# Performance work log

Measured on AMD Instinct MI355X. Metric: run time of the kernel, lower is better.

The kernel has to match this reference:

```python
import jax, jax.numpy as jnp
import numpy as np

N, IN, C, H = 16384, 64, 4, 16
MAXS = 16  # upper bound on squaring steps (norms here give s ~ 7-8)


def setup_inputs() -> dict:
    key = jax.random.key(0)
    k1, k2, k3 = jax.random.split(key, 3)
    dX = jax.random.normal(k1, (N, IN), dtype=jnp.float32)
    Ar = jax.random.normal(k2, (IN, C, H, H), dtype=jnp.float32)
    Ai = jax.random.normal(k3, (IN, C, H, H), dtype=jnp.float32)
    return {"dX": dX, "Ar": Ar, "Ai": Ai}


def reference(dX, Ar, Ai):
    # Parameter A as complex64, projected onto the unitary Lie algebra (skew-Hermitian)
    A = (Ar + 1j * Ai).astype(jnp.complex64)
    A = (A - jnp.conj(jnp.swapaxes(A, -2, -1))) * 0.5  # (IN, C, H, H)
    # AX[n,c,i,j] = sum_k A[k,c,i,j] * dX[n,k]  -> (N, C, H, H)
    AX = jnp.einsum('kcij,nk->ncij', A, dX.astype(jnp.complex64))
    # induced 1-norm: max over columns of column abs-sums
    normA = jnp.max(jnp.sum(jnp.abs(AX), axis=-2), axis=-1)  # (N, C), real
    s = jnp.where(normA > 1, jnp.ceil(jnp.log2(normA)), 0.0).astype(jnp.int32)
    # scaling: exp(A) = exp(A / 2^s) ^ (2^s); integer s detaches grad like torch .long()
    scale = jnp.exp2(-s.astype(jnp.float32)).astype(jnp.complex64)[..., None, None]
    A1 = AX * scale
    n, c, h, _ = A1.shape
    P = jax.vmap(jax.scipy.linalg.expm)(A1.reshape(-1, h, h)).reshape(n, c, h, h)
    # repeated squaring, masked per (n, c) element; fixed trip count for jit
    for i in range(MAXS):
        P = jnp.where((s > i)[..., None, None], P @ P, P)
    return P
```

## Files before the change

### kernel.cpp

```cpp
#include <hip/hip_runtime.h>
#include <math.h>

#define NN       16384
#define IN_DIM   64
#define CC       4
#define NMAT     (NN * CC)

#define C0 1.0f
#define C1 1.0f
#define C2 0.5f
#define C3 0.16666666666666666f
#define C4 0.041666666666666664f
#define C5 0.008333333333333333f
#define C6 0.001388888888888889f
#define C7 1.984126984126984e-4f
#define C8 2.48015873015873e-5f

typedef __attribute__((ext_vector_type(8))) short bf16x8;
typedef __attribute__((ext_vector_type(4))) float f32x4;

#define MFMA16(A, B, C) __builtin_amdgcn_mfma_f32_16x16x32_bf16((A), (B), (C), 0, 0, 0)

#define COLP   768
#define ROWB   3072
#define MATB   6144
#define WPB    4

__device__ __forceinline__ unsigned hi16(float x) {
    return __builtin_bit_cast(unsigned, x) >> 16;
}
__device__ __forceinline__ float hif(float x) {
    return __builtin_bit_cast(float, __builtin_bit_cast(unsigned, x) & 0xFFFF0000u);
}
__device__ __forceinline__ unsigned pk2(float a, float b) {
    return (__builtin_bit_cast(unsigned, a) >> 16) |
           (__builtin_bit_cast(unsigned, b) & 0xFFFF0000u);
}

__global__ __launch_bounds__(256)
void ax_kernel(const float* __restrict__ dX, const float* __restrict__ Ar,
               const float* __restrict__ Ai, float* __restrict__ ws)
{
    const int t  = threadIdx.x;
    const int nb = blockIdx.x * 8;
    const int c  = t >> 6;
    const int i  = (t >> 2) & 15;
    const int j0 = (t & 3) * 4;

    float accre[8][4], accim[8][4];
#pragma unroll
    for (int nn_ = 0; nn_ < 8; ++nn_)
#pragma unroll
        for (int jj = 0; jj < 4; ++jj) { accre[nn_][jj] = 0.f; accim[nn_][jj] = 0.f; }

#pragma unroll 2
    for (int k = 0; k < IN_DIM; ++k) {
        const int base = (k * CC + c) * 256 + i * 16 + j0;
        const float4 ar = *reinterpret_cast<const float4*>(Ar + base);
        const float4 ai = *reinterpret_cast<const float4*>(Ai + base);
#pragma unroll
        for (int nn_ = 0; nn_ < 8; ++nn_) {
            const float dxv = dX[(nb + nn_) * IN_DIM + k];
#pragma unroll
            for (int jj = 0; jj < 4; ++jj) {
                accre[nn_][jj] = fmaf(dxv, (&ar.x)[jj], accre[nn_][jj]);
                accim[nn_][jj] = fmaf(dxv, (&ai.x)[jj], accim[nn_][jj]);
            }
        }
    }
#pragma unroll
    for (int nn_ = 0; nn_ < 8; ++nn_) {
        const int m = (nb + nn_) * CC + c;
        float* o = ws + (size_t)m * 512 + (i * 16 + j0) * 2;
        reinterpret_cast<float4*>(o)[0] =
            make_float4(accre[nn_][0], accim[nn_][0], accre[nn_][1], accim[nn_][1]);
        reinterpret_cast<float4*>(o)[1] =
            make_float4(accre[nn_][2], accim[nn_][2], accre[nn_][3], accim[nn_][3]);
    }
}

__global__ __launch_bounds__(256)
void expm_mfma_kernel(const float* __restrict__ dX, const float* __restrict__ Ar,
                      const float* __restrict__ Ai, const float* __restrict__ ws,
                      float* __restrict__ out, const int use_ws, const int real_only)
{
    __shared__ __align__(16) unsigned char ldsraw[WPB * MATB];

    const int t = threadIdx.x;
    const int w = t >> 6;
    const int l = t & 63;
    unsigned char* L = ldsraw + w * MATB;

    const int m  = blockIdx.x * WPB + w;
    const int n  = m >> 2;
    const int cc = m & 3;

    const int c     = l & 15;
    const int g     = l >> 4;
    const int ghalf = g & 1;
    const int gsel  = g >> 1;

    const int colent  = c * 48 + ghalf * 16;
    const int off_B1h = (gsel ? COLP : 0) + colent;
    const int off_B2h = (gsel ? 0 : COLP) + colent;
    const int off_Ah  = ROWB + (gsel ? COLP : 0) + colent;
    const int wc      = c * 48 + g * 8;

    const short ns = gsel ? (short)0x8000 : (short)0;
    const bf16x8 negv = {ns, ns, ns, ns, ns, ns, ns, ns};

    float dq[4];
#pragma unroll
    for (int q = 0; q < 4; ++q) dq[q] = ((4 * g + q) == c) ? 1.f : 0.f;

    float aRe[4], aIm[4];
    if (use_ws) {
        const float* gp = ws + (size_t)m * 512;
#pragma unroll
        for (int q = 0; q < 4; ++q) {
            const int r = 4 * g + q;
            const float2 v = *reinterpret_cast<const float2*>(gp + (r * 16 + c) * 2);
            const float2 u = *reinterpret_cast<const float2*>(gp + (c * 16 + r) * 2);
            aRe[q] = 0.5f * (v.x - u.x);
            aIm[q] = 0.5f * (v.y + u.y);
        }
    } else {
        float bRe[4] = {0,0,0,0}, bIm[4] = {0,0,0,0}, uRe[4] = {0,0,0,0}, uIm[4] = {0,0,0,0};
        for (int k = 0; k < IN_DIM; ++k) {
            const float dxv = dX[n * IN_DIM + k];
            const int base = (k * CC + cc) * 256;
#pragma unroll
            for (int q = 0; q < 4; ++q) {
                const int r = 4 * g + q;
                bRe[q] = fmaf(dxv, Ar[base + r * 16 + c], bRe[q]);
                bIm[q] = fmaf(dxv, Ai[base + r * 16 + c], bIm[q]);
                uRe[q] = fmaf(dxv, Ar[base + c * 16 + r], uRe[q]);
                uIm[q] = fmaf(dxv, Ai[base + c * 16 + r], uIm[q]);
            }
        }
#pragma unroll
        for (int q = 0; q < 4; ++q) {
            aRe[q] = 0.5f * (bRe[q] - uRe[q]);
            aIm[q] = 0.5f * (bIm[q] + uIm[q]);
        }
    }

    float colsum = 0.f;
#pragma unroll
    for (int q = 0; q < 4; ++q)
        colsum += sqrtf(aRe[q] * aRe[q] + aIm[q] * aIm[q]);
    colsum += __shfl_xor(colsum, 16);
    colsum += __shfl_xor(colsum, 32);
    float mx = colsum;
    mx = fmaxf(mx, __shfl_xor(mx, 1));
    mx = fmaxf(mx, __shfl_xor(mx, 2));
    mx = fmaxf(mx, __shfl_xor(mx, 4));
    mx = fmaxf(mx, __shfl_xor(mx, 8));

    int s = 0;
    if (mx > 1.f) s = (int)ceilf(log2f(mx));
    if (s < 0) s = 0;
    if (s > 16) s = 16;
    const float sc = exp2f((float)(-s));
#pragma unroll
    for (int q = 0; q < 4; ++q) { aRe[q] *= sc; aIm[q] *= sc; }

    auto wcol = [&](const float* vR, const float* vI) {
        uint2 xh, yh, xl, yl;
        xh.x = pk2(vR[0], vR[1]); xh.y = pk2(vR[2], vR[3]);
        yh.x = pk2(vI[0], vI[1]); yh.y = pk2(vI[2], vI[3]);
        float l0 = vR[0] - hif(vR[0]), l1 = vR[1] - hif(vR[1]);
        float l2 = vR[2] - hif(vR[2]), l3 = vR[3] - hif(vR[3]);
        xl.x = pk2(l0, l1); xl.y = pk2(l2, l3);
        l0 = vI[0] - hif(vI[0]); l1 = vI[1] - hif(vI[1]);
        l2 = vI[2] - hif(vI[2]); l3 = vI[3] - hif(vI[3]);
        yl.x = pk2(l0, l1); yl.y = pk2(l2, l3);
        *reinterpret_cast<uint2*>(L + 0    + wc) = xh;
        *reinterpret_cast<uint2*>(L + COLP + wc) = yh;
        *reinterpret_cast<uint2*>(L + 1536 + wc) = xl;
        *reinterpret_cast<uint2*>(L + 2304 + wc) = yl;
    };
    auto wrow = [&](const float* vR, const float* vI) {
#pragma unroll
        for (int q = 0; q < 4; ++q) {
            const int rb = ROWB + (4 * g + q) * 48 + c * 2;
            *reinterpret_cast<unsigned short*>(L + rb + 0)    = (unsigned short)hi16(vR[q]);
            *reinterpret_cast<unsigned short*>(L + rb + COLP) = (unsigned short)hi16(vI[q]);
            const float lr = vR[q] - hif(vR[q]);
            const float li = vI[q] - hif(vI[q]);
            *reinterpret_cast<unsigned short*>(L + rb + 1536) = (unsigned short)hi16(lr);
            *reinterpret_cast<unsigned short*>(L + rb + 2304) = (unsigned short)hi16(li);
        }
    };
    auto cmul = [&](const bf16x8 Ah, const bf16x8 Al, f32x4& accRe, f32x4& accIm) {
        bf16x8 b1h = *reinterpret_cast<const bf16x8*>(L + off_B1h);
        bf16x8 b1l = *reinterpret_cast<const bf16x8*>(L + off_B1h + 1536);
        const bf16x8 b2h = *reinterpret_cast<const bf16x8*>(L + off_B2h);
        const bf16x8 b2l = *reinterpret_cast<const bf16x8*>(L + off_B2h + 1536);
        b1h ^= negv;
        b1l ^= negv;
        accRe = MFMA16(Ah, b1h, accRe);
        accRe = MFMA16(Ah, b1l, accRe);
        accRe = MFMA16(Al, b1h, accRe);
        accIm = MFMA16(Ah, b2h, accIm);
        accIm = MFMA16(Ah, b2l, accIm);
        accIm = MFMA16(Al, b2h, accIm);
    };

    wcol(aRe, aIm);
    wrow(aRe, aIm);
    bf16x8 Ah = *reinterpret_cast<const bf16x8*>(L + off_Ah);
    bf16x8 Al = *reinterpret_cast<const bf16x8*>(L + off_Ah + 1536);
    f32x4 zr4 = {0.f, 0.f, 0.f, 0.f}, zi4 = {0.f, 0.f, 0.f, 0.f};
    cmul(Ah, Al, zr4, zi4);

    float zr[4], zi[4];
#pragma unroll
    for (int q = 0; q < 4; ++q) { zr[q] = zr4[q]; zi[q] = zi4[q]; }
    wrow(zr, zi);
    const bf16x8 ZAh = *reinterpret_cast<const bf16x8*>(L + off_Ah);
    const bf16x8 ZAl = *reinterpret_cast<const bf16x8*>(L + off_Ah + 1536);

    float tRe[4], tIm[4];
#pragma unroll
    for (int q = 0; q < 4; ++q) {
        tRe[q] = C8 * zr[q] + C7 * aRe[q] + C6 * dq[q];
        tIm[q] = C8 * zi[q] + C7 * aIm[q];
    }

    const float cE[3] = {C4, C2, C0};
    const float cO[3] = {C5, C3, C1};
#pragma unroll
    for (int h = 0; h < 3; ++h) {
        wcol(tRe, tIm);
        f32x4 rr, ri;
#pragma unroll
        for (int q = 0; q < 4; ++q) {
            rr[q] = cO[h] * aRe[q] + cE[h] * dq[q];
            ri[q] = cO[h] * aIm[q];
        }
        cmul(ZAh, ZAl, rr, ri);
#pragma unroll
        for (int q = 0; q < 4; ++q) { tRe[q] = rr[q]; tIm[q] = ri[q]; }
    }

#pragma unroll 1
    for (int it = 0; it < s; ++it) {
        wcol(tRe, tIm);
        wrow(tRe, tIm);
        const bf16x8 Ph = *reinterpret_cast<const bf16x8*>(L + off_Ah);
        const bf16x8 Pl = *reinterpret_cast<const bf16x8*>(L + off_Ah + 1536);
        f32x4 rr = {0.f, 0.f, 0.f, 0.f}, ri = {0.f, 0.f, 0.f, 0.f};
        cmul(Ph, Pl, rr, ri);
#pragma unroll
        for (int q = 0; q < 4; ++q) { tRe[q] = rr[q]; tIm[q] = ri[q]; }
    }

    if (real_only) {
        float* po = out + (size_t)m * 256;
#pragma unroll
        for (int q = 0; q < 4; ++q)
            po[(4 * g + q) * 16 + c] = tRe[q];
    } else {
        float* po = out + (size_t)m * 512;
#pragma unroll
        for (int q = 0; q < 4; ++q)
            *reinterpret_cast<float2*>(po + ((4 * g + q) * 16 + c) * 2) =
                make_float2(tRe[q], tIm[q]);
    }
}

extern "C" void kernel_launch(void* const* d_in, const int* in_sizes, int n_in,
                              void* d_out, int out_size, void* d_ws, size_t ws_size,
                              hipStream_t stream)
{
    const float* dX = (const float*)d_in[0];
    const float* Ar = (const float*)d_in[1];
    const float* Ai = (const float*)d_in[2];
    float* out = (float*)d_out;
    float* ws  = (float*)d_ws;

    const int real_only = (out_size < NMAT * 512) ? 1 : 0;
    const size_t need = (size_t)NMAT * 512 * sizeof(float);
    const int use_ws = (ws_size >= need) ? 1 : 0;

    if (use_ws)
        hipLaunchKernelGGL(ax_kernel, dim3(NN / 8), dim3(256), 0, stream, dX, Ar, Ai, ws);
    hipLaunchKernelGGL(expm_mfma_kernel, dim3(NMAT / WPB), dim3(256), 0, stream,
                       dX, Ar, Ai, ws, out, use_ws, real_only);
}
```

Baseline: 258.3 us.

## Replace LDS operand staging with wave shuffles and track conjugate-transpose for squaring

Removes the per-wave LDS buffer. MFMA A/B operands are now built with cross-lane shuffles from register-packed bf16 hi/lo pieces. Because the input is skew-Hermitian, the kernel also evaluates the Taylor polynomial at -A to get exp(A)^H. During squaring it keeps both P and P^H so each operand comes from the right layout without a transpose through memory. This doubles the polynomial MFMA work and adds many shuffles and selects per step, in exchange for removing LDS stores, loads and bank traffic. It also skips the imaginary part on the last step when only real output is needed.

```diff
diff --git a/kernel.cpp b/kernel.cpp
--- a/kernel.cpp
+++ b/kernel.cpp
@@ -20,15 +20,8 @@
 typedef __attribute__((ext_vector_type(4))) float f32x4;
 
 #define MFMA16(A, B, C) __builtin_amdgcn_mfma_f32_16x16x32_bf16((A), (B), (C), 0, 0, 0)
-
-#define COLP   768
-#define ROWB   3072
-#define MATB   6144
-#define WPB    4
-
-__device__ __forceinline__ unsigned hi16(float x) {
-    return __builtin_bit_cast(unsigned, x) >> 16;
-}
+#define SHF(x, src) ((unsigned)__shfl((int)(x), (src)))
+
 __device__ __forceinline__ float hif(float x) {
     return __builtin_bit_cast(float, __builtin_bit_cast(unsigned, x) & 0xFFFF0000u);
 }
@@ -84,30 +77,21 @@
                       const float* __restrict__ Ai, const float* __restrict__ ws,
                       float* __restrict__ out, const int use_ws, const int real_only)
 {
-    __shared__ __align__(16) unsigned char ldsraw[WPB * MATB];
-
     const int t = threadIdx.x;
     const int w = t >> 6;
     const int l = t & 63;
-    unsigned char* L = ldsraw + w * MATB;
-
-    const int m  = blockIdx.x * WPB + w;
+
+    const int m  = blockIdx.x * 4 + w;
     const int n  = m >> 2;
     const int cc = m & 3;
 
-    const int c     = l & 15;
-    const int g     = l >> 4;
-    const int ghalf = g & 1;
-    const int gsel  = g >> 1;
-
-    const int colent  = c * 48 + ghalf * 16;
-    const int off_B1h = (gsel ? COLP : 0) + colent;
-    const int off_B2h = (gsel ? 0 : COLP) + colent;
-    const int off_Ah  = ROWB + (gsel ? COLP : 0) + colent;
-    const int wc      = c * 48 + g * 8;
-
-    const short ns = gsel ? (short)0x8000 : (short)0;
-    const bf16x8 negv = {ns, ns, ns, ns, ns, ns, ns, ns};
+    const int c  = l & 15;
+    const int g  = l >> 4;
+    const int gh = g & 1;
+    const bool gs = (g >= 2);
+    const int s0 = 32 * gh + c;
+    const int s1 = s0 + 16;
+    const unsigned SG = 0x80008000u;
 
     float dq[4];
 #pragma unroll
@@ -157,116 +141,166 @@
     mx = fmaxf(mx, __shfl_xor(mx, 4));
     mx = fmaxf(mx, __shfl_xor(mx, 8));
 
-    int s = 0;
-    if (mx > 1.f) s = (int)ceilf(log2f(mx));
-    if (s < 0) s = 0;
-    if (s > 16) s = 16;
-    const float sc = exp2f((float)(-s));
+    int s_ = 0;
+    if (mx > 1.f) s_ = (int)ceilf(log2f(mx));
+    if (s_ < 0) s_ = 0;
+    if (s_ > 16) s_ = 16;
+    const float sc = exp2f((float)(-s_));
 #pragma unroll
     for (int q = 0; q < 4; ++q) { aRe[q] *= sc; aIm[q] *= sc; }
 
-    auto wcol = [&](const float* vR, const float* vI) {
-        uint2 xh, yh, xl, yl;
-        xh.x = pk2(vR[0], vR[1]); xh.y = pk2(vR[2], vR[3]);
-        yh.x = pk2(vI[0], vI[1]); yh.y = pk2(vI[2], vI[3]);
-        float l0 = vR[0] - hif(vR[0]), l1 = vR[1] - hif(vR[1]);
-        float l2 = vR[2] - hif(vR[2]), l3 = vR[3] - hif(vR[3]);
-        xl.x = pk2(l0, l1); xl.y = pk2(l2, l3);
-        l0 = vI[0] - hif(vI[0]); l1 = vI[1] - hif(vI[1]);
-        l2 = vI[2] - hif(vI[2]); l3 = vI[3] - hif(vI[3]);
-        yl.x = pk2(l0, l1); yl.y = pk2(l2, l3);
-        *reinterpret_cast<uint2*>(L + 0    + wc) = xh;
-        *reinterpret_cast<uint2*>(L + COLP + wc) = yh;
-        *reinterpret_cast<uint2*>(L + 1536 + wc) = xl;
-        *reinterpret_cast<uint2*>(L + 2304 + wc) = yl;
+    auto pack4 = [&](const float* vR, const float* vI,
+                     unsigned* xh, unsigned* xl, unsigned* yh, unsigned* yl) {
+#pragma unroll
+        for (int p = 0; p < 2; ++p) {
+            xh[p] = pk2(vR[2 * p], vR[2 * p + 1]);
+            yh[p] = pk2(vI[2 * p], vI[2 * p + 1]);
+            xl[p] = pk2(vR[2 * p] - hif(vR[2 * p]), vR[2 * p + 1] - hif(vR[2 * p + 1]));
+            yl[p] = pk2(vI[2 * p] - hif(vI[2 * p]), vI[2 * p + 1] - hif(vI[2 * p + 1]));
+        }
     };
-    auto wrow = [&](const float* vR, const float* vI) {
-#pragma unroll
-        for (int q = 0; q < 4; ++q) {
-            const int rb = ROWB + (4 * g + q) * 48 + c * 2;
-            *reinterpret_cast<unsigned short*>(L + rb + 0)    = (unsigned short)hi16(vR[q]);
-            *reinterpret_cast<unsigned short*>(L + rb + COLP) = (unsigned short)hi16(vI[q]);
-            const float lr = vR[q] - hif(vR[q]);
-            const float li = vI[q] - hif(vI[q]);
-            *reinterpret_cast<unsigned short*>(L + rb + 1536) = (unsigned short)hi16(lr);
-            *reinterpret_cast<unsigned short*>(L + rb + 2304) = (unsigned short)hi16(li);
-        }
+    auto bset = [&](const unsigned* xh, const unsigned* xl,
+                    const unsigned* yh, const unsigned* yl,
+                    unsigned* Px, unsigned* PxL, unsigned* Py, unsigned* PyL) {
+        Px[0]  = SHF(xh[0], s0); Px[1]  = SHF(xh[1], s0); Px[2]  = SHF(xh[0], s1); Px[3]  = SHF(xh[1], s1);
+        PxL[0] = SHF(xl[0], s0); PxL[1] = SHF(xl[1], s0); PxL[2] = SHF(xl[0], s1); PxL[3] = SHF(xl[1], s1);
+        Py[0]  = SHF(yh[0], s0); Py[1]  = SHF(yh[1], s0); Py[2]  = SHF(yh[0], s1); Py[3]  = SHF(yh[1], s1);
+        PyL[0] = SHF(yl[0], s0); PyL[1] = SHF(yl[1], s0); PyL[2] = SHF(yl[0], s1); PyL[3] = SHF(yl[1], s1);
     };
-    auto cmul = [&](const bf16x8 Ah, const bf16x8 Al, f32x4& accRe, f32x4& accIm) {
-        bf16x8 b1h = *reinterpret_cast<const bf16x8*>(L + off_B1h);
-        bf16x8 b1l = *reinterpret_cast<const bf16x8*>(L + off_B1h + 1536);
-        const bf16x8 b2h = *reinterpret_cast<const bf16x8*>(L + off_B2h);
-        const bf16x8 b2l = *reinterpret_cast<const bf16x8*>(L + off_B2h + 1536);
-        b1h ^= negv;
-        b1l ^= negv;
-        accRe = MFMA16(Ah, b1h, accRe);
-        accRe = MFMA16(Ah, b1l, accRe);
-        accRe = MFMA16(Al, b1h, accRe);
-        accIm = MFMA16(Ah, b2h, accIm);
-        accIm = MFMA16(Ah, b2l, accIm);
-        accIm = MFMA16(Al, b2h, accIm);
+    auto sel4 = [&](const unsigned* X, const unsigned* Y, unsigned sx, unsigned sy) -> bf16x8 {
+        union { unsigned u[4]; bf16x8 v; } r;
+#pragma unroll
+        for (int i = 0; i < 4; ++i) r.u[i] = gs ? (Y[i] ^ sy) : (X[i] ^ sx);
+        return r.v;
     };
 
-    wcol(aRe, aIm);
-    wrow(aRe, aIm);
-    bf16x8 Ah = *reinterpret_cast<const bf16x8*>(L + off_Ah);
-    bf16x8 Al = *reinterpret_cast<const bf16x8*>(L + off_Ah + 1536);
+    unsigned AXh[2], AXl[2], AYh[2], AYl[2];
+    pack4(aRe, aIm, AXh, AXl, AYh, AYl);
+    unsigned Pxh[4], Pxl[4], Pyh[4], Pyl[4];
+    bset(AXh, AXl, AYh, AYl, Pxh, Pxl, Pyh, Pyl);
+
+    {
+    }
+    bf16x8 fh  = sel4(Pxh, Pyh, SG, 0);
+    bf16x8 fl  = sel4(Pxl, Pyl, SG, 0);
+    bf16x8 b1h = sel4(Pxh, Pyh, 0, SG);
+    bf16x8 b1l = sel4(Pxl, Pyl, 0, SG);
+    bf16x8 b2h = sel4(Pyh, Pxh, 0, 0);
+    bf16x8 b2l = sel4(Pyl, Pxl, 0, 0);
     f32x4 zr4 = {0.f, 0.f, 0.f, 0.f}, zi4 = {0.f, 0.f, 0.f, 0.f};
-    cmul(Ah, Al, zr4, zi4);
+    zr4 = MFMA16(fh, b1h, zr4); zr4 = MFMA16(fh, b1l, zr4); zr4 = MFMA16(fl, b1h, zr4);
+    zi4 = MFMA16(fh, b2h, zi4); zi4 = MFMA16(fh, b2l, zi4); zi4 = MFMA16(fl, b2h, zi4);
 
     float zr[4], zi[4];
 #pragma unroll
     for (int q = 0; q < 4; ++q) { zr[q] = zr4[q]; zi[q] = zi4[q]; }
-    wrow(zr, zi);
-    const bf16x8 ZAh = *reinterpret_cast<const bf16x8*>(L + off_Ah);
-    const bf16x8 ZAl = *reinterpret_cast<const bf16x8*>(L + off_Ah + 1536);
-
-    float tRe[4], tIm[4];
+
+    unsigned ZXh[2], ZXl[2], ZYh[2], ZYl[2];
+    pack4(zr, zi, ZXh, ZXl, ZYh, ZYl);
+    {
+        unsigned Qxh[4], Qxl[4], Qyh[4], Qyl[4];
+        bset(ZXh, ZXl, ZYh, ZYl, Qxh, Qxl, Qyh, Qyl);
+        fh = sel4(Qxh, Qyh, 0, SG);
+        fl = sel4(Qxl, Qyl, 0, SG);
+    }
+    const bf16x8 zfh = fh, zfl = fl;
+
+    float tR[4], tI[4], sR[4], sI[4];
 #pragma unroll
     for (int q = 0; q < 4; ++q) {
-        tRe[q] = C8 * zr[q] + C7 * aRe[q] + C6 * dq[q];
-        tIm[q] = C8 * zi[q] + C7 * aIm[q];
+        tR[q] = C8 * zr[q] + C7 * aRe[q] + C6 * dq[q];
+        tI[q] = C8 * zi[q] + C7 * aIm[q];
+        sR[q] = C8 * zr[q] - C7 * aRe[q] + C6 * dq[q];
+        sI[q] = C8 * zi[q] - C7 * aIm[q];
     }
 
     const float cE[3] = {C4, C2, C0};
     const float cO[3] = {C5, C3, C1};
 #pragma unroll
     for (int h = 0; h < 3; ++h) {
-        wcol(tRe, tIm);
-        f32x4 rr, ri;
+        unsigned TXh[2], TXl[2], TYh[2], TYl[2];
+        pack4(tR, tI, TXh, TXl, TYh, TYl);
+        bset(TXh, TXl, TYh, TYl, Pxh, Pxl, Pyh, Pyl);
+        b1h = sel4(Pxh, Pyh, 0, SG); b1l = sel4(Pxl, Pyl, 0, SG);
+        b2h = sel4(Pyh, Pxh, 0, 0);  b2l = sel4(Pyl, Pxl, 0, 0);
+        f32x4 ar = {cO[h] * aRe[0] + cE[h] * dq[0], cO[h] * aRe[1] + cE[h] * dq[1],
+                    cO[h] * aRe[2] + cE[h] * dq[2], cO[h] * aRe[3] + cE[h] * dq[3]};
+        f32x4 ai = {cO[h] * aIm[0], cO[h] * aIm[1], cO[h] * aIm[2], cO[h] * aIm[3]};
+        ar = MFMA16(zfh, b1h, ar); ar = MFMA16(zfh, b1l, ar); ar = MFMA16(zfl, b1h, ar);
+        ai = MFMA16(zfh, b2h, ai); ai = MFMA16(zfh, b2l, ai); ai = MFMA16(zfl, b2h, ai);
+
+        pack4(sR, sI, TXh, TXl, TYh, TYl);
+        bset(TXh, TXl, TYh, TYl, Pxh, Pxl, Pyh, Pyl);
+        b1h = sel4(Pxh, Pyh, 0, SG); b1l = sel4(Pxl, Pyl, 0, SG);
+        b2h = sel4(Pyh, Pxh, 0, 0);  b2l = sel4(Pyl, Pxl, 0, 0);
+        f32x4 br = {-cO[h] * aRe[0] + cE[h] * dq[0], -cO[h] * aRe[1] + cE[h] * dq[1],
+                    -cO[h] * aRe[2] + cE[h] * dq[2], -cO[h] * aRe[3] + cE[h] * dq[3]};
+        f32x4 bi = {-cO[h] * aIm[0], -cO[h] * aIm[1], -cO[h] * aIm[2], -cO[h] * aIm[3]};
+        br = MFMA16(zfh, b1h, br); br = MFMA16(zfh, b1l, br); br = MFMA16(zfl, b1h, br);
+        bi = MFMA16(zfh, b2h, bi); bi = MFMA16(zfh, b2l, bi); bi = MFMA16(zfl, b2h, bi);
+
 #pragma unroll
         for (int q = 0; q < 4; ++q) {
-            rr[q] = cO[h] * aRe[q] + cE[h] * dq[q];
-            ri[q] = cO[h] * aIm[q];
-        }
-        cmul(ZAh, ZAl, rr, ri);
-#pragma unroll
-        for (int q = 0; q < 4; ++q) { tRe[q] = rr[q]; tIm[q] = ri[q]; }
-    }
+            tR[q] = ar[q]; tI[q] = ai[q];
+            sR[q] = br[q]; sI[q] = bi[q];
+        }
+    }
+
+    float uR[4], uI[4];
+#pragma unroll
+    for (int q = 0; q < 4; ++q) { uR[q] = sR[q]; uI[q] = -sI[q]; }
 
 #pragma unroll 1
-    for (int it = 0; it < s; ++it) {
-        wcol(tRe, tIm);
-        wrow(tRe, tIm);
-        const bf16x8 Ph = *reinterpret_cast<const bf16x8*>(L + off_Ah);
-        const bf16x8 Pl = *reinterpret_cast<const bf16x8*>(L + off_Ah + 1536);
-        f32x4 rr = {0.f, 0.f, 0.f, 0.f}, ri = {0.f, 0.f, 0.f, 0.f};
-        cmul(Ph, Pl, rr, ri);
-#pragma unroll
-        for (int q = 0; q < 4; ++q) { tRe[q] = rr[q]; tIm[q] = ri[q]; }
+    for (int it = 0; it < s_; ++it) {
+        unsigned TXh[2], TXl[2], TYh[2], TYl[2];
+        unsigned UXh[2], UXl[2], UYh[2], UYl[2];
+        pack4(tR, tI, TXh, TXl, TYh, TYl);
+        pack4(uR, uI, UXh, UXl, UYh, UYl);
+        unsigned Qxh[4], Qxl[4], Qyh[4], Qyl[4];
+        bset(TXh, TXl, TYh, TYl, Pxh, Pxl, Pyh, Pyl);
+        bset(UXh, UXl, UYh, UYl, Qxh, Qxl, Qyh, Qyl);
+
+        const bf16x8 afh = sel4(Qxh, Qyh, 0, 0);
+        const bf16x8 afl = sel4(Qxl, Qyl, 0, 0);
+        b1h = sel4(Pxh, Pyh, 0, SG); b1l = sel4(Pxl, Pyl, 0, SG);
+        f32x4 r = {0.f, 0.f, 0.f, 0.f};
+        r = MFMA16(afh, b1h, r); r = MFMA16(afh, b1l, r); r = MFMA16(afl, b1h, r);
+        const bool needIm = !(real_only && (it == s_ - 1));
+        f32x4 i4 = {0.f, 0.f, 0.f, 0.f};
+        if (needIm) {
+            b2h = sel4(Pyh, Pxh, 0, 0); b2l = sel4(Pyl, Pxl, 0, 0);
+            i4 = MFMA16(afh, b2h, i4); i4 = MFMA16(afh, b2l, i4); i4 = MFMA16(afl, b2h, i4);
+        }
+
+        if (it < s_ - 1) {
+            const bf16x8 a2h = sel4(Pxh, Pyh, 0, 0);
+            const bf16x8 a2l = sel4(Pxl, Pyl, 0, 0);
+            const bf16x8 c1h = sel4(Qxh, Qyh, 0, SG), c1l = sel4(Qxl, Qyl, 0, SG);
+            const bf16x8 c2h = sel4(Qyh, Qxh, 0, 0),  c2l = sel4(Qyl, Qxl, 0, 0);
+            f32x4 ur = {0.f, 0.f, 0.f, 0.f}, ui = {0.f, 0.f, 0.f, 0.f};
+            ur = MFMA16(a2h, c1h, ur); ur = MFMA16(a2h, c1l, ur); ur = MFMA16(a2l, c1h, ur);
+            ui = MFMA16(a2h, c2h, ui); ui = MFMA16(a2h, c2l, ui); ui = MFMA16(a2l, c2h, ui);
+#pragma unroll
+            for (int q = 0; q < 4; ++q) { uR[q] = ur[q]; uI[q] = ui[q]; }
+        }
+#pragma unroll
+        for (int q = 0; q < 4; ++q) {
+            tR[q] = r[q];
+            if (needIm) tI[q] = i4[q];
+        }
     }
 
     if (real_only) {
         float* po = out + (size_t)m * 256;
 #pragma unroll
         for (int q = 0; q < 4; ++q)
-            po[(4 * g + q) * 16 + c] = tRe[q];
+            po[(4 * g + q) * 16 + c] = tR[q];
     } else {
         float* po = out + (size_t)m * 512;
 #pragma unroll
         for (int q = 0; q < 4; ++q)
             *reinterpret_cast<float2*>(po + ((4 * g + q) * 16 + c) * 2) =
-                make_float2(tRe[q], tIm[q]);
+                make_float2(tR[q], tI[q]);
     }
 }
 
@@ -286,6 +320,6 @@
 
     if (use_ws)
         hipLaunchKernelGGL(ax_kernel, dim3(NN / 8), dim3(256), 0, stream, dX, Ar, Ai, ws);
-    hipLaunchKernelGGL(expm_mfma_kernel, dim3(NMAT / WPB), dim3(256), 0, stream,
+    hipLaunchKernelGGL(expm_mfma_kernel, dim3(NMAT / 4), dim3(256), 0, stream,
                        dX, Ar, Ai, ws, out, use_ws, real_only);
 }
```

After: 351.2 us. 36.0% more time.
